# Optimization experiments

Hardware: AMD Instinct MI355X
Metric: run time of the kernel (lower is better)

Reference implementation:

```python
import jax, jax.numpy as jnp
import numpy as np

B, T, C = 4, 2048, 1024
H = 16
D = C // H  # 64


def setup_inputs() -> dict:
    key = jax.random.key(0)
    ks = jax.random.split(key, 5)
    scale = 0.02
    x = jax.random.normal(ks[0], (B, T, C), dtype=jnp.float32)
    # Linear weights stored in [in, out] layout (equivalent to torch W.T)
    W_qkv = jax.random.normal(ks[1], (C, 3 * C), dtype=jnp.float32) * scale
    b_qkv = jax.random.normal(ks[2], (3 * C,), dtype=jnp.float32) * scale
    W_out = jax.random.normal(ks[3], (C, C), dtype=jnp.float32) * scale
    b_out = jax.random.normal(ks[4], (C,), dtype=jnp.float32) * scale
    return {"x": x, "W_qkv": W_qkv, "b_qkv": b_qkv, "W_out": W_out, "b_out": b_out}


def reference(x, W_qkv, b_qkv, W_out, b_out):
    Bx, Tx, Cx = x.shape
    qkv = x @ W_qkv + b_qkv                      # [B,T,3C]
    qkv = qkv.reshape(Bx, Tx, 3, H, D)
    q = jnp.transpose(qkv[:, :, 0], (0, 2, 1, 3))  # [B,H,T,D]
    k = jnp.transpose(qkv[:, :, 1], (0, 2, 1, 3))
    v = jnp.transpose(qkv[:, :, 2], (0, 2, 1, 3))
    scores = jnp.einsum('bhqd,bhkd->bhqk', q, k) / jnp.sqrt(jnp.float32(D))
    causal = jnp.tril(jnp.ones((Tx, Tx), dtype=bool))  # keep lower triangle
    scores = jnp.where(causal, scores, jnp.float32(-jnp.inf))
    w = jax.nn.softmax(scores, axis=-1)           # dropout p=0.0 (eval)
    out = jnp.einsum('bhqk,bhkd->bhqd', w, v)     # [B,H,T,D]
    out = jnp.transpose(out, (0, 2, 1, 3)).reshape(Bx, Tx, Cx)
    return out @ W_out + b_out
```

## Files before the change

kernel.cpp:

```cpp
#include <hip/hip_runtime.h>

typedef _Float16 f16;
typedef _Float16 f16x4 __attribute__((ext_vector_type(4)));
typedef _Float16 f16x8 __attribute__((ext_vector_type(8)));
typedef float    f32x4 __attribute__((ext_vector_type(4)));

#define B_ 4
#define T_ 2048
#define C_ 1024
#define H_ 16
#define D_ 64

__device__ __forceinline__ void gload_lds16(const f16* g, f16* l) {
  __builtin_amdgcn_global_load_lds(
      (const __attribute__((address_space(1))) unsigned int*)g,
      (__attribute__((address_space(3))) unsigned int*)l, 16, 0, 0);
}

__global__ void cvt_kernel(const float* __restrict__ in, f16* __restrict__ out, int n4) {
  int i = blockIdx.x * blockDim.x + threadIdx.x;
  int stride = gridDim.x * blockDim.x;
  for (; i < n4; i += stride) {
    float4 v = ((const float4*)in)[i];
    f16x4 h = { (f16)v.x, (f16)v.y, (f16)v.z, (f16)v.w };
    ((f16x4*)out)[i] = h;
  }
}

__global__ void transpose_cvt_kernel(const float* __restrict__ W, f16* __restrict__ Wt,
                                     int K, int N) {
  __shared__ f16 tile[32][33];
  int bx = blockIdx.x, by = blockIdx.y;
  int tx = threadIdx.x & 31, ty = threadIdx.x >> 5;
  #pragma unroll
  for (int i = ty; i < 32; i += 8)
    tile[i][tx] = (f16)W[(size_t)(by * 32 + i) * N + bx * 32 + tx];
  __syncthreads();
  #pragma unroll
  for (int i = ty; i < 32; i += 8)
    Wt[(size_t)(bx * 32 + i) * K + by * 32 + tx] = tile[tx][i];
}

__global__ __launch_bounds__(512, 2)
void gemm256_kernel(const f16* __restrict__ A, const f16* __restrict__ Bt,
                    const float* __restrict__ bias,
                    f16* __restrict__ q, f16* __restrict__ kk, f16* __restrict__ vt) {
  const int M_ = 8192, N_ = 3072, K_ = 1024;
  __shared__ __align__(16) f16 As[2][2][128 * 64];
  __shared__ __align__(16) f16 Bs[2][2][128 * 64];

  const int bid = blockIdx.x;
  const int wg = (bid & 7) * 48 + (bid >> 3);
  const int bm = wg / 12, bn = wg % 12;
  const int m0 = bm << 8, n0 = bn << 8;
  const int lane = threadIdx.x & 63, wid = threadIdx.x >> 6;
  const int wm = wid >> 2;
  const int bhalf = (wid >> 1) & 1;
  const int brow0 = (wid & 1) << 6;
  const int rr = lane & 15, g = lane >> 4;
  const int swz = (rr & 4) << 3;

  f32x4 acc[8][4] = {};

  const int srow = (wid << 3) + (lane >> 3);
  const int scol = ((((lane & 7) << 4) ^ (lane & 32)) >> 1);
  const f16* Abase = A + (size_t)(m0 + srow) * K_ + scol;
  const f16* Bbase = Bt + (size_t)(n0 + srow) * K_ + scol;

  auto STAGE_A = [&](int buf, int half, int tile) {
    #pragma unroll
    for (int c = 0; c < 2; ++c)
      gload_lds16(Abase + (size_t)(half * 128 + c * 64) * K_ + tile * 64,
                  &As[buf][half][c * 4096 + wid * 512]);
  };
  auto STAGE_B = [&](int buf, int half, int tile) {
    #pragma unroll
    for (int c = 0; c < 2; ++c)
      gload_lds16(Bbase + (size_t)(half * 128 + c * 64) * K_ + tile * 64,
                  &Bs[buf][half][c * 4096 + wid * 512]);
  };

  auto LDA = [&](int buf, int mhalf, int kkk, f16x8* af) {
    #pragma unroll
    for (int f = 0; f < 4; ++f)
      af[f] = *(const f16x8*)((const char*)&As[buf][wm][0]
               + (mhalf * 64 + f * 16 + rr) * 128 + ((kkk * 64 + g * 16) ^ swz));
  };
  auto LDB = [&](int buf, int kkk, f16x8* bf) {
    #pragma unroll
    for (int nf = 0; nf < 4; ++nf)
      bf[nf] = *(const f16x8*)((const char*)&Bs[buf][bhalf][0]
               + (brow0 + nf * 16 + rr) * 128 + ((kkk * 64 + g * 16) ^ swz));
  };

  #define BAR() { __builtin_amdgcn_s_barrier(); __builtin_amdgcn_sched_barrier(0); }
  #define MMA(MH, AF, BF) { \
    __builtin_amdgcn_s_setprio(1); \
    _Pragma("unroll") \
    for (int f = 0; f < 4; ++f) \
      _Pragma("unroll") \
      for (int nf = 0; nf < 4; ++nf) \
        acc[(MH) * 4 + f][nf] = \
            __builtin_amdgcn_mfma_f32_16x16x32_f16(AF[f], BF[nf], acc[(MH) * 4 + f][nf], 0, 0, 0); \
    __builtin_amdgcn_s_setprio(0); }

  STAGE_A(0, 0, 0); STAGE_A(0, 1, 0);
  STAGE_B(0, 0, 0); STAGE_B(0, 1, 0);
  STAGE_B(1, 0, 1);
  asm volatile("s_waitcnt vmcnt(2)" ::: "memory");
  BAR();

  const int NT = 16;
  #pragma unroll 1
  for (int i = 0; i < 8; ++i) {
    const int t1 = 2 * i + 1, t2 = 2 * i + 2, t3 = 2 * i + 3;
    f16x8 af[4], bf[4];
    LDB(0, 0, bf); LDA(0, 0, 0, af);
    STAGE_B(1, 1, t1);
    BAR(); MMA(0, af, bf); BAR();
    LDA(0, 1, 0, af);
    STAGE_A(1, 0, t1);
    BAR(); MMA(1, af, bf); BAR();
    LDB(0, 1, bf); LDA(0, 0, 1, af);
    STAGE_A(1, 1, t1);
    BAR(); MMA(0, af, bf); BAR();
    LDA(0, 1, 1, af);
    if (t2 < NT) {
      STAGE_B(0, 0, t2);
      asm volatile("s_waitcnt vmcnt(2)" ::: "memory");
    } else {
      asm volatile("s_waitcnt vmcnt(0)" ::: "memory");
    }
    BAR(); MMA(1, af, bf); BAR();
    LDB(1, 0, bf); LDA(1, 0, 0, af);
    if (t2 < NT) STAGE_B(0, 1, t2);
    BAR(); MMA(0, af, bf); BAR();
    LDA(1, 1, 0, af);
    if (t2 < NT) STAGE_A(0, 0, t2);
    BAR(); MMA(1, af, bf); BAR();
    LDB(1, 1, bf); LDA(1, 0, 1, af);
    if (t2 < NT) STAGE_A(0, 1, t2);
    BAR(); MMA(0, af, bf); BAR();
    LDA(1, 1, 1, af);
    if (t3 < NT) {
      STAGE_B(1, 0, t3);
      asm volatile("s_waitcnt vmcnt(2)" ::: "memory");
    } else if (i < 7) {
      asm volatile("s_waitcnt vmcnt(0)" ::: "memory");
    }
    BAR(); MMA(1, af, bf); BAR();
  }
  #undef MMA
  #undef BAR

  const int col = lane & 15;
  const int row4 = (lane >> 4) << 2;
  const int seg = n0 >> 10;
  #pragma unroll
  for (int mi = 0; mi < 8; ++mi) {
    #pragma unroll
    for (int nf = 0; nf < 4; ++nf) {
      const int n = n0 + (wid & 3) * 64 + nf * 16 + col;
      const float bn_ = bias[n];
      const int cc = n & 1023;
      const int h = cc >> 6, d = cc & 63;
      #pragma unroll
      for (int r = 0; r < 4; ++r) {
        const int m = m0 + wm * 128 + mi * 16 + row4 + r;
        const float v = acc[mi][nf][r] + bn_;
        const int b = m >> 11, t = m & 2047;
        const size_t bh = (size_t)b * 16 + h;
        const f16 hv = (f16)v;
        if (seg == 0)      q [(bh * T_ + t) * D_ + d] = hv;
        else if (seg == 1) kk[(bh * T_ + t) * D_ + d] = hv;
        else               vt[(bh * D_ + d) * T_ + t] = hv;
      }
    }
  }
}

__global__ __launch_bounds__(256, 3)
void gemm_kernel(const f16* __restrict__ A, const f16* __restrict__ Bt,
                 const float* __restrict__ bias, float* __restrict__ outF,
                 int M, int N, int K) {
  __shared__ __align__(16) f16 As[3][128 * 32];
  __shared__ __align__(16) f16 Bs[3][128 * 32];
  const int nbn = N >> 7;
  const int bid = blockIdx.x;
  const int bm = bid / nbn, bn = bid % nbn;
  const int m0 = bm << 7, n0 = bn << 7;
  const int tid = threadIdx.x;
  const int lane = tid & 63, wid = tid >> 6;
  const int wr = wid >> 1, wc = wid & 1;

  f32x4 acc[4][4] = {};

  const int srow = lane >> 2;
  const int scol = (lane & 3) << 3;
  const f16* Abase = A + (size_t)(m0 + srow) * K + scol;
  const f16* Bbase = Bt + (size_t)(n0 + srow) * K + scol;

  auto stage = [&](int buf, int kt) {
    const int c0 = wid * 2;
    #pragma unroll
    for (int c = c0; c < c0 + 2; ++c) {
      gload_lds16(Abase + (size_t)c * 16 * K + kt * 32, &As[buf][c * 512]);
      gload_lds16(Bbase + (size_t)c * 16 * K + kt * 32, &Bs[buf][c * 512]);
    }
  };

  const int ko = (lane >> 4) << 3;
  const int rr = lane & 15;

  auto compute = [&](int buf) {
    f16x8 af[4], bf[4];
    #pragma unroll
    for (int t = 0; t < 4; ++t) {
      af[t] = *(const f16x8*)&As[buf][(wr * 64 + t * 16 + rr) * 32 + ko];
      bf[t] = *(const f16x8*)&Bs[buf][(wc * 64 + t * 16 + rr) * 32 + ko];
    }
    __builtin_amdgcn_s_setprio(1);
    #pragma unroll
    for (int i = 0; i < 4; ++i)
      #pragma unroll
      for (int j = 0; j < 4; ++j)
        acc[i][j] = __builtin_amdgcn_mfma_f32_16x16x32_f16(af[i], bf[j], acc[i][j], 0, 0, 0);
    __builtin_amdgcn_s_setprio(0);
  };

  const int nk = K >> 5;
  int bcur = 0, bnext = 1, bnn = 2;
  stage(0, 0);
  stage(1, 1);
  asm volatile("s_waitcnt vmcnt(4)" ::: "memory");
  __builtin_amdgcn_s_barrier();
  __builtin_amdgcn_sched_barrier(0);
  for (int t = 0; t < nk; ++t) {
    if (t + 2 < nk) stage(bnn, t + 2);
    compute(bcur);
    if (t + 1 < nk) {
      if (t + 2 < nk) asm volatile("s_waitcnt vmcnt(4)" ::: "memory");
      else            asm volatile("s_waitcnt vmcnt(0)" ::: "memory");
      __builtin_amdgcn_s_barrier();
      __builtin_amdgcn_sched_barrier(0);
    }
    const int tmp = bcur; bcur = bnext; bnext = bnn; bnn = tmp;
  }

  const int col = lane & 15;
  const int row4 = (lane >> 4) << 2;
  #pragma unroll
  for (int i = 0; i < 4; ++i) {
    #pragma unroll
    for (int j = 0; j < 4; ++j) {
      const int n = n0 + wc * 64 + j * 16 + col;
      const float bn_ = bias[n];
      #pragma unroll
      for (int r = 0; r < 4; ++r) {
        const int m = m0 + wr * 64 + i * 16 + row4 + r;
        outF[(size_t)m * N + n] = acc[i][j][r] + bn_;
      }
    }
  }
}

__global__ __launch_bounds__(512, 2)
void attn_kernel(const f16* __restrict__ Q, const f16* __restrict__ Kg,
                 const f16* __restrict__ Vt, f16* __restrict__ Aout) {
  __shared__ __align__(16) f16 Ks[2][64 * 64];
  __shared__ __align__(16) f16 Vs[2][64 * 64];
  __shared__ __align__(16) f16 Pt[8][16][72];

  const int bid = blockIdx.x;
  const int wgid = (bid & 7) * 128 + (bid >> 3);
  const int bh = wgid >> 4;
  const int ti = 15 - (wgid & 15);
  const int lane = threadIdx.x & 63, w = threadIdx.x >> 6;
  const int col = lane & 15;
  const int g = lane >> 4;
  const int ko = g << 3;

  const f16* Qp = Q + (size_t)bh * T_ * D_;
  const f16* Kp = Kg + (size_t)bh * T_ * D_;
  const f16* Vp = Vt + (size_t)bh * D_ * T_;

  const int srow8 = lane >> 3;
  const int scb = ((lane & 7) << 4) ^ (srow8 << 4);
  const int krow_s = (w << 3) + srow8;

  auto stage = [&](int buf, int kb) {
    gload_lds16(Kp + (size_t)(kb + krow_s) * D_ + (scb >> 1), &Ks[buf][w * 512]);
    gload_lds16(Vp + (size_t)krow_s * T_ + kb + (scb >> 1), &Vs[buf][w * 512]);
  };
  auto ldsK = [&](int buf, int krow, int d0) -> f16x8 {
    const int off = krow * 128 + ((d0 << 1) ^ ((krow & 7) << 4));
    return *(const f16x8*)((const char*)&Ks[buf][0] + off);
  };
  auto ldsV = [&](int buf, int drow, int k0) -> f16x8 {
    const int off = drow * 128 + ((k0 << 1) ^ ((drow & 7) << 4));
    return *(const f16x8*)((const char*)&Vs[buf][0] + off);
  };

  const int q0 = ti << 7;
  const int qrow0 = q0 + (w << 4);
  const int nkt = (ti << 1) + 2;
  const int qg = qrow0 + col;

  f16x8 qf[2];
  #pragma unroll
  for (int s = 0; s < 2; ++s) {
    f16x8 t = *(const f16x8*)&Qp[(size_t)qg * D_ + s * 32 + ko];
    #pragma unroll
    for (int e = 0; e < 8; ++e) t[e] = t[e] * (f16)0.125f;
    qf[s] = t;
  }

  f32x4 o[4] = {};
  float m = -1e30f, l = 0.f;

  stage(0, 0);
  __syncthreads();
  int cur = 0;
  for (int kt = 0; kt < nkt; ++kt) {
    const int kb = kt << 6;
    if (kt + 1 < nkt) stage(cur ^ 1, (kt + 1) << 6);

    if (kb <= qrow0 + 15) {
      f32x4 sc[4] = {};
      #pragma unroll
      for (int s = 0; s < 2; ++s)
        #pragma unroll
        for (int mt = 0; mt < 4; ++mt) {
          f16x8 kf = ldsK(cur, mt * 16 + col, s * 32 + ko);
          sc[mt] = __builtin_amdgcn_mfma_f32_16x16x32_f16(kf, qf[s], sc[mt], 0, 0, 0);
        }

      const bool needMask = (kb + 63 > qrow0);
      if (needMask) {
        #pragma unroll
        for (int mt = 0; mt < 4; ++mt)
          #pragma unroll
          for (int r = 0; r < 4; ++r)
            if (kb + mt * 16 + (g << 2) + r > qg) sc[mt][r] = -1e30f;
      }

      float mx = fmaxf(fmaxf(fmaxf(sc[0][0], sc[0][1]), fmaxf(sc[0][2], sc[0][3])),
                       fmaxf(fmaxf(sc[1][0], sc[1][1]), fmaxf(sc[1][2], sc[1][3])));
      mx = fmaxf(mx, fmaxf(fmaxf(fmaxf(sc[2][0], sc[2][1]), fmaxf(sc[2][2], sc[2][3])),
                           fmaxf(fmaxf(sc[3][0], sc[3][1]), fmaxf(sc[3][2], sc[3][3]))));
      mx = fmaxf(mx, __shfl_xor(mx, 16, 64));
      mx = fmaxf(mx, __shfl_xor(mx, 32, 64));

      if (!__all(mx - m <= 8.f)) {
        const float mnew = fmaxf(m, mx);
        const float alpha = __expf(m - mnew);
        m = mnew;
        l *= alpha;
        #pragma unroll
        for (int mt = 0; mt < 4; ++mt)
          #pragma unroll
          for (int r = 0; r < 4; ++r) o[mt][r] *= alpha;
      }

      float rs = 0.f;
      #pragma unroll
      for (int mt = 0; mt < 4; ++mt) {
        f16x4 ph;
        #pragma unroll
        for (int r = 0; r < 4; ++r) {
          const float p = __expf(sc[mt][r] - m);
          rs += p;
          ph[r] = (f16)p;
        }
        *(f16x4*)&Pt[w][col][mt * 16 + (g << 2)] = ph;
      }
      rs += __shfl_xor(rs, 16, 64);
      rs += __shfl_xor(rs, 32, 64);
      l += rs;

      #pragma unroll
      for (int s = 0; s < 2; ++s) {
        f16x8 pb = *(const f16x8*)&Pt[w][col][s * 32 + ko];
        #pragma unroll
        for (int mt = 0; mt < 4; ++mt) {
          f16x8 vf = ldsV(cur, mt * 16 + col, s * 32 + ko);
          o[mt] = __builtin_amdgcn_mfma_f32_16x16x32_f16(vf, pb, o[mt], 0, 0, 0);
        }
      }
    }

    __syncthreads();
    cur ^= 1;
  }

  const int b = bh >> 4, h = bh & 15;
  const float inv = 1.0f / l;
  const size_t rowoff = ((size_t)b * T_ + qg) * C_ + (size_t)h * D_;
  #pragma unroll
  for (int mt = 0; mt < 4; ++mt) {
    f16x4 ov;
    #pragma unroll
    for (int r = 0; r < 4; ++r) ov[r] = (f16)(o[mt][r] * inv);
    *(f16x4*)&Aout[rowoff + mt * 16 + (g << 2)] = ov;
  }
}

extern "C" void kernel_launch(void* const* d_in, const int* in_sizes, int n_in,
                              void* d_out, int out_size, void* d_ws, size_t ws_size,
                              hipStream_t stream) {
  const float* x    = (const float*)d_in[0];
  const float* Wqkv = (const float*)d_in[1];
  const float* bqkv = (const float*)d_in[2];
  const float* Wout = (const float*)d_in[3];
  const float* bout = (const float*)d_in[4];
  float* out = (float*)d_out;

  char* ws = (char*)d_ws;
  f16* xb     = (f16*)ws;
  f16* Wqkv_t = (f16*)(ws + (16u << 20));
  f16* Wout_t = (f16*)(ws + (22u << 20));
  f16* Qb     = (f16*)(ws + (24u << 20));
  f16* Kb     = (f16*)(ws + (40u << 20));
  f16* Vtb    = (f16*)(ws + (56u << 20));

  cvt_kernel<<<2048, 256, 0, stream>>>(x, xb, (B_ * T_ * C_) / 4);
  dim3 g1(3072 / 32, 1024 / 32);
  transpose_cvt_kernel<<<g1, 256, 0, stream>>>(Wqkv, Wqkv_t, 1024, 3072);
  dim3 g2(1024 / 32, 1024 / 32);
  transpose_cvt_kernel<<<g2, 256, 0, stream>>>(Wout, Wout_t, 1024, 1024);

  gemm256_kernel<<<384, 512, 0, stream>>>(xb, Wqkv_t, bqkv, Qb, Kb, Vtb);
  attn_kernel<<<1024, 512, 0, stream>>>(Qb, Kb, Vtb, xb );
  gemm_kernel<<<64 * 8, 256, 0, stream>>>(xb, Wout_t, bout, out, 8192, 1024, 1024);
}
```

Before: 229.2 us.

## Restructure attention into paired causal tiles with 32-row waves and triple buffering

The attention kernel now uses 256-thread blocks in which each wave handles 32 query rows, so every K/V fragment read from LDS feeds two MFMAs. Each block processes a short and a long causal tile pair (pr and 15-pr) to balance work, and K/V staging moves to a three-buffer pipeline with explicit vmcnt waits. Separately, the LDS swizzles in both GEMM kernels are changed to XOR-based patterns meant to reduce bank conflicts. In exchange the attention kernel needs more registers per wave and launches half as many blocks.

```diff
diff --git a/kernel.cpp b/kernel.cpp
--- a/kernel.cpp
+++ b/kernel.cpp
@@ -45,7 +45,7 @@
 void gemm256_kernel(const f16* __restrict__ A, const f16* __restrict__ Bt,
                     const float* __restrict__ bias,
                     f16* __restrict__ q, f16* __restrict__ kk, f16* __restrict__ vt) {
-  const int M_ = 8192, N_ = 3072, K_ = 1024;
+  const int K_ = 1024;
   __shared__ __align__(16) f16 As[2][2][128 * 64];
   __shared__ __align__(16) f16 Bs[2][2][128 * 64];
 
@@ -58,12 +58,11 @@
   const int bhalf = (wid >> 1) & 1;
   const int brow0 = (wid & 1) << 6;
   const int rr = lane & 15, g = lane >> 4;
-  const int swz = (rr & 4) << 3;
 
   f32x4 acc[8][4] = {};
 
   const int srow = (wid << 3) + (lane >> 3);
-  const int scol = ((((lane & 7) << 4) ^ (lane & 32)) >> 1);
+  const int scol = (((lane & 7) ^ ((lane >> 3) & 7)) << 3);
   const f16* Abase = A + (size_t)(m0 + srow) * K_ + scol;
   const f16* Bbase = Bt + (size_t)(n0 + srow) * K_ + scol;
 
@@ -84,13 +83,15 @@
     #pragma unroll
     for (int f = 0; f < 4; ++f)
       af[f] = *(const f16x8*)((const char*)&As[buf][wm][0]
-               + (mhalf * 64 + f * 16 + rr) * 128 + ((kkk * 64 + g * 16) ^ swz));
+               + (mhalf * 64 + f * 16 + rr) * 128
+               + ((kkk * 64 + g * 16) ^ ((rr & 7) << 4)));
   };
   auto LDB = [&](int buf, int kkk, f16x8* bf) {
     #pragma unroll
     for (int nf = 0; nf < 4; ++nf)
       bf[nf] = *(const f16x8*)((const char*)&Bs[buf][bhalf][0]
-               + (brow0 + nf * 16 + rr) * 128 + ((kkk * 64 + g * 16) ^ swz));
+               + (brow0 + nf * 16 + rr) * 128
+               + ((kkk * 64 + g * 16) ^ ((rr & 7) << 4)));
   };
 
   #define BAR() { __builtin_amdgcn_s_barrier(); __builtin_amdgcn_sched_barrier(0); }
@@ -196,7 +197,7 @@
   f32x4 acc[4][4] = {};
 
   const int srow = lane >> 2;
-  const int scol = (lane & 3) << 3;
+  const int scol = (((lane & 3) ^ ((lane >> 2) & 3)) << 3);
   const f16* Abase = A + (size_t)(m0 + srow) * K + scol;
   const f16* Bbase = Bt + (size_t)(n0 + srow) * K + scol;
 
@@ -209,15 +210,16 @@
     }
   };
 
-  const int ko = (lane >> 4) << 3;
+  const int g = lane >> 4;
   const int rr = lane & 15;
+  const int swz = (g ^ (rr & 3)) << 4;
 
   auto compute = [&](int buf) {
     f16x8 af[4], bf[4];
     #pragma unroll
     for (int t = 0; t < 4; ++t) {
-      af[t] = *(const f16x8*)&As[buf][(wr * 64 + t * 16 + rr) * 32 + ko];
-      bf[t] = *(const f16x8*)&Bs[buf][(wc * 64 + t * 16 + rr) * 32 + ko];
+      af[t] = *(const f16x8*)((const char*)&As[buf][0] + (wr * 64 + t * 16 + rr) * 64 + swz);
+      bf[t] = *(const f16x8*)((const char*)&Bs[buf][0] + (wc * 64 + t * 16 + rr) * 64 + swz);
     }
     __builtin_amdgcn_s_setprio(1);
     #pragma unroll
@@ -264,17 +266,17 @@
   }
 }
 
-__global__ __launch_bounds__(512, 2)
+__global__ __launch_bounds__(256, 2)
 void attn_kernel(const f16* __restrict__ Q, const f16* __restrict__ Kg,
                  const f16* __restrict__ Vt, f16* __restrict__ Aout) {
-  __shared__ __align__(16) f16 Ks[2][64 * 64];
-  __shared__ __align__(16) f16 Vs[2][64 * 64];
-  __shared__ __align__(16) f16 Pt[8][16][72];
+  __shared__ __align__(16) f16 Ks[3][64 * 64];
+  __shared__ __align__(16) f16 Vs[3][64 * 64];
+  __shared__ __align__(16) f16 Pt[4][32 * 64];
 
   const int bid = blockIdx.x;
-  const int wgid = (bid & 7) * 128 + (bid >> 3);
-  const int bh = wgid >> 4;
-  const int ti = 15 - (wgid & 15);
+  const int wgid = (bid & 7) * 64 + (bid >> 3);
+  const int bh = wgid >> 3;
+  const int pr = wgid & 7;
   const int lane = threadIdx.x & 63, w = threadIdx.x >> 6;
   const int col = lane & 15;
   const int g = lane >> 4;
@@ -284,13 +286,16 @@
   const f16* Kp = Kg + (size_t)bh * T_ * D_;
   const f16* Vp = Vt + (size_t)bh * D_ * T_;
 
-  const int srow8 = lane >> 3;
-  const int scb = ((lane & 7) << 4) ^ (srow8 << 4);
-  const int krow_s = (w << 3) + srow8;
+  const int sr = lane >> 3;
+  const int sc = ((lane & 7) ^ (sr & 7)) << 3;
 
   auto stage = [&](int buf, int kb) {
-    gload_lds16(Kp + (size_t)(kb + krow_s) * D_ + (scb >> 1), &Ks[buf][w * 512]);
-    gload_lds16(Vp + (size_t)krow_s * T_ + kb + (scb >> 1), &Vs[buf][w * 512]);
+    #pragma unroll
+    for (int c2 = 0; c2 < 2; ++c2) {
+      const int c = (w << 1) + c2;
+      gload_lds16(Kp + (size_t)(kb + (c << 3) + sr) * D_ + sc, &Ks[buf][c * 512]);
+      gload_lds16(Vp + (size_t)((c << 3) + sr) * T_ + kb + sc, &Vs[buf][c * 512]);
+    }
   };
   auto ldsK = [&](int buf, int krow, int d0) -> f16x8 {
     const int off = krow * 128 + ((d0 << 1) ^ ((krow & 7) << 4));
@@ -301,107 +306,143 @@
     return *(const f16x8*)((const char*)&Vs[buf][0] + off);
   };
 
-  const int q0 = ti << 7;
-  const int qrow0 = q0 + (w << 4);
-  const int nkt = (ti << 1) + 2;
-  const int qg = qrow0 + col;
-
-  f16x8 qf[2];
-  #pragma unroll
-  for (int s = 0; s < 2; ++s) {
-    f16x8 t = *(const f16x8*)&Qp[(size_t)qg * D_ + s * 32 + ko];
-    #pragma unroll
-    for (int e = 0; e < 8; ++e) t[e] = t[e] * (f16)0.125f;
-    qf[s] = t;
-  }
-
-  f32x4 o[4] = {};
-  float m = -1e30f, l = 0.f;
-
-  stage(0, 0);
-  __syncthreads();
-  int cur = 0;
-  for (int kt = 0; kt < nkt; ++kt) {
-    const int kb = kt << 6;
-    if (kt + 1 < nkt) stage(cur ^ 1, (kt + 1) << 6);
-
-    if (kb <= qrow0 + 15) {
-      f32x4 sc[4] = {};
+  char* PtW = (char*)&Pt[w][0];
+  const int b = bh >> 4, hd = bh & 15;
+
+  #pragma unroll 1
+  for (int tt = 0; tt < 2; ++tt) {
+    const int ti = tt ? (15 - pr) : pr;
+    const int qrow0 = (ti << 7) + (w << 5);
+    const int nkt = (ti << 1) + 2;
+
+    f16x8 qf[2][2];
+    #pragma unroll
+    for (int h = 0; h < 2; ++h)
       #pragma unroll
-      for (int s = 0; s < 2; ++s)
-        #pragma unroll
-        for (int mt = 0; mt < 4; ++mt) {
-          f16x8 kf = ldsK(cur, mt * 16 + col, s * 32 + ko);
-          sc[mt] = __builtin_amdgcn_mfma_f32_16x16x32_f16(kf, qf[s], sc[mt], 0, 0, 0);
+      for (int s = 0; s < 2; ++s) {
+        f16x8 t = *(const f16x8*)&Qp[(size_t)(qrow0 + h * 16 + col) * D_ + s * 32 + ko];
+        #pragma unroll
+        for (int e = 0; e < 8; ++e) t[e] = t[e] * (f16)0.125f;
+        qf[h][s] = t;
+      }
+
+    f32x4 o[2][4] = {};
+    float m[2] = {-1e30f, -1e30f}, l[2] = {0.f, 0.f};
+
+    int b0 = 0, b1 = 1, b2 = 2;
+    stage(b0, 0);
+    stage(b1, 64);
+    asm volatile("s_waitcnt vmcnt(4)" ::: "memory");
+    __builtin_amdgcn_s_barrier();
+    __builtin_amdgcn_sched_barrier(0);
+
+    for (int kt = 0; kt < nkt; ++kt) {
+      const int kb = kt << 6;
+      if (kt + 2 < nkt) stage(b2, kb + 128);
+
+      if (kb <= qrow0 + 31) {
+        f32x4 sc2[2][4] = {};
+        #pragma unroll
+        for (int s = 0; s < 2; ++s)
+          #pragma unroll
+          for (int mt = 0; mt < 4; ++mt) {
+            f16x8 kf = ldsK(b0, mt * 16 + col, s * 32 + ko);
+            sc2[0][mt] = __builtin_amdgcn_mfma_f32_16x16x32_f16(kf, qf[0][s], sc2[0][mt], 0, 0, 0);
+            sc2[1][mt] = __builtin_amdgcn_mfma_f32_16x16x32_f16(kf, qf[1][s], sc2[1][mt], 0, 0, 0);
+          }
+
+        if (kb + 63 > qrow0) {
+          #pragma unroll
+          for (int mt = 0; mt < 4; ++mt)
+            #pragma unroll
+            for (int r = 0; r < 4; ++r) {
+              const int kv = kb + mt * 16 + (g << 2) + r;
+              if (kv > qrow0 + col)      sc2[0][mt][r] = -1e30f;
+              if (kv > qrow0 + 16 + col) sc2[1][mt][r] = -1e30f;
+            }
         }
 
-      const bool needMask = (kb + 63 > qrow0);
-      if (needMask) {
-        #pragma unroll
-        for (int mt = 0; mt < 4; ++mt)
+        float mx[2];
+        #pragma unroll
+        for (int h = 0; h < 2; ++h) {
+          float v = fmaxf(fmaxf(fmaxf(sc2[h][0][0], sc2[h][0][1]), fmaxf(sc2[h][0][2], sc2[h][0][3])),
+                          fmaxf(fmaxf(sc2[h][1][0], sc2[h][1][1]), fmaxf(sc2[h][1][2], sc2[h][1][3])));
+          v = fmaxf(v, fmaxf(fmaxf(fmaxf(sc2[h][2][0], sc2[h][2][1]), fmaxf(sc2[h][2][2], sc2[h][2][3])),
+                             fmaxf(fmaxf(sc2[h][3][0], sc2[h][3][1]), fmaxf(sc2[h][3][2], sc2[h][3][3]))));
+          v = fmaxf(v, __shfl_xor(v, 16, 64));
+          v = fmaxf(v, __shfl_xor(v, 32, 64));
+          mx[h] = v;
+        }
+
+        if (!__all(fmaxf(mx[0] - m[0], mx[1] - m[1]) <= 8.f)) {
           #pragma unroll
-          for (int r = 0; r < 4; ++r)
-            if (kb + mt * 16 + (g << 2) + r > qg) sc[mt][r] = -1e30f;
+          for (int h = 0; h < 2; ++h) {
+            const float mnew = fmaxf(m[h], mx[h]);
+            const float alpha = __expf(m[h] - mnew);
+            m[h] = mnew;
+            l[h] *= alpha;
+            #pragma unroll
+            for (int mt = 0; mt < 4; ++mt)
+              #pragma unroll
+              for (int r = 0; r < 4; ++r) o[h][mt][r] *= alpha;
+          }
+        }
+
+        #pragma unroll
+        for (int h = 0; h < 2; ++h) {
+          float rs = 0.f;
+          #pragma unroll
+          for (int mt = 0; mt < 4; ++mt) {
+            f16x4 ph;
+            #pragma unroll
+            for (int r = 0; r < 4; ++r) {
+              const float p = __expf(sc2[h][mt][r] - m[h]);
+              rs += p;
+              ph[r] = (f16)p;
+            }
+            *(f16x4*)(PtW + (h * 16 + col) * 128 + (((mt << 5) + (g << 3)) ^ ((col & 7) << 4))) = ph;
+          }
+          rs += __shfl_xor(rs, 16, 64);
+          rs += __shfl_xor(rs, 32, 64);
+          l[h] += rs;
+        }
+
+        #pragma unroll
+        for (int s = 0; s < 2; ++s) {
+          const int pcb = ((s << 6) + (g << 4)) ^ ((col & 7) << 4);
+          f16x8 pb0 = *(const f16x8*)(PtW + col * 128 + pcb);
+          f16x8 pb1 = *(const f16x8*)(PtW + (16 + col) * 128 + pcb);
+          #pragma unroll
+          for (int mt = 0; mt < 4; ++mt) {
+            f16x8 vf = ldsV(b0, mt * 16 + col, s * 32 + ko);
+            o[0][mt] = __builtin_amdgcn_mfma_f32_16x16x32_f16(vf, pb0, o[0][mt], 0, 0, 0);
+            o[1][mt] = __builtin_amdgcn_mfma_f32_16x16x32_f16(vf, pb1, o[1][mt], 0, 0, 0);
+          }
+        }
       }
 
-      float mx = fmaxf(fmaxf(fmaxf(sc[0][0], sc[0][1]), fmaxf(sc[0][2], sc[0][3])),
-                       fmaxf(fmaxf(sc[1][0], sc[1][1]), fmaxf(sc[1][2], sc[1][3])));
-      mx = fmaxf(mx, fmaxf(fmaxf(fmaxf(sc[2][0], sc[2][1]), fmaxf(sc[2][2], sc[2][3])),
-                           fmaxf(fmaxf(sc[3][0], sc[3][1]), fmaxf(sc[3][2], sc[3][3]))));
-      mx = fmaxf(mx, __shfl_xor(mx, 16, 64));
-      mx = fmaxf(mx, __shfl_xor(mx, 32, 64));
-
-      if (!__all(mx - m <= 8.f)) {
-        const float mnew = fmaxf(m, mx);
-        const float alpha = __expf(m - mnew);
-        m = mnew;
-        l *= alpha;
-        #pragma unroll
-        for (int mt = 0; mt < 4; ++mt)
-          #pragma unroll
-          for (int r = 0; r < 4; ++r) o[mt][r] *= alpha;
-      }
-
-      float rs = 0.f;
+      __builtin_amdgcn_sched_barrier(0);
+      if (kt + 2 < nkt) asm volatile("s_waitcnt vmcnt(4)" ::: "memory");
+      else              asm volatile("s_waitcnt vmcnt(0)" ::: "memory");
+      __builtin_amdgcn_s_barrier();
+      __builtin_amdgcn_sched_barrier(0);
+      const int tmp = b0; b0 = b1; b1 = b2; b2 = tmp;
+    }
+
+    #pragma unroll
+    for (int h = 0; h < 2; ++h) {
+      const float inv = 1.0f / l[h];
+      const int t = qrow0 + h * 16 + col;
+      const size_t rowoff = ((size_t)b * T_ + t) * C_ + (size_t)hd * D_;
       #pragma unroll
       for (int mt = 0; mt < 4; ++mt) {
-        f16x4 ph;
-        #pragma unroll
-        for (int r = 0; r < 4; ++r) {
-          const float p = __expf(sc[mt][r] - m);
-          rs += p;
-          ph[r] = (f16)p;
-        }
-        *(f16x4*)&Pt[w][col][mt * 16 + (g << 2)] = ph;
+        f16x4 ov;
+        #pragma unroll
+        for (int r = 0; r < 4; ++r) ov[r] = (f16)(o[h][mt][r] * inv);
+        *(f16x4*)&Aout[rowoff + mt * 16 + (g << 2)] = ov;
       }
-      rs += __shfl_xor(rs, 16, 64);
-      rs += __shfl_xor(rs, 32, 64);
-      l += rs;
-
-      #pragma unroll
-      for (int s = 0; s < 2; ++s) {
-        f16x8 pb = *(const f16x8*)&Pt[w][col][s * 32 + ko];
-        #pragma unroll
-        for (int mt = 0; mt < 4; ++mt) {
-          f16x8 vf = ldsV(cur, mt * 16 + col, s * 32 + ko);
-          o[mt] = __builtin_amdgcn_mfma_f32_16x16x32_f16(vf, pb, o[mt], 0, 0, 0);
-        }
-      }
-    }
-
-    __syncthreads();
-    cur ^= 1;
-  }
-
-  const int b = bh >> 4, h = bh & 15;
-  const float inv = 1.0f / l;
-  const size_t rowoff = ((size_t)b * T_ + qg) * C_ + (size_t)h * D_;
-  #pragma unroll
-  for (int mt = 0; mt < 4; ++mt) {
-    f16x4 ov;
-    #pragma unroll
-    for (int r = 0; r < 4; ++r) ov[r] = (f16)(o[mt][r] * inv);
-    *(f16x4*)&Aout[rowoff + mt * 16 + (g << 2)] = ov;
+    }
+    __builtin_amdgcn_s_barrier();
   }
 }
 
@@ -430,6 +471,6 @@
   transpose_cvt_kernel<<<g2, 256, 0, stream>>>(Wout, Wout_t, 1024, 1024);
 
   gemm256_kernel<<<384, 512, 0, stream>>>(xb, Wqkv_t, bqkv, Qb, Kb, Vtb);
-  attn_kernel<<<1024, 512, 0, stream>>>(Qb, Kb, Vtb, xb );
+  attn_kernel<<<512, 256, 0, stream>>>(Qb, Kb, Vtb, xb );
   gemm_kernel<<<64 * 8, 256, 0, stream>>>(xb, Wout_t, bout, out, 8192, 1024, 1024);
 }
```

Result: faster. 210.8 us (-8.0%).
